# Kernel tuning notes

Measured on AMD Instinct MI355X. Metric: run time of the kernel, lower is better.

## Reference

```python
import jax, jax.numpy as jnp
import numpy as np

BITWIDTH = 8
T = 1 << BITWIDTH  # 256 bit-clock cycles
N = 262144         # independent bitstreams


def _sobol_1d(dim, n=T, out_bits=BITWIDTH):
    """One coordinate of an n-point Sobol sequence (Joe-Kuo dirs), scaled to [0, 2^out_bits)."""
    L = 30
    if dim == 1:
        v = [1 << (L - 1 - j) for j in range(L)]  # van der Corput
    else:
        params = {2: (1, 0, [1]), 3: (2, 1, [1, 3]), 4: (3, 1, [1, 3, 1])}
        s, a, m = params[dim]
        vv = [0] * (L + 1)
        for j in range(1, s + 1):
            vv[j] = m[j - 1] << (L - j)
        for j in range(s + 1, L + 1):
            vj = vv[j - s] ^ (vv[j - s] >> s)
            for k in range(1, s):
                if (a >> (s - 1 - k)) & 1:
                    vj ^= vv[j - k]
            vv[j] = vj
        v = vv[1:]
    x = np.zeros(n, dtype=np.int64)
    for i in range(1, n):
        acc, ii, j = 0, i, 0
        while ii:
            if ii & 1:
                acc ^= v[j]
            ii >>= 1
            j += 1
        x[i] = acc
    return (x >> (L - out_bits)).astype(np.float32)  # integers in [0, 256)


def _const_bitstream(value, rng_dim):
    """BSGen(SourceGen(value)): bit[t] = (round(value*2^B) > sobol_rng[t])."""
    src = np.round(value * (1 << BITWIDTH)).astype(np.float32)
    rng = _sobol_1d(rng_dim)
    return jnp.asarray((src > rng).astype(np.float32))


def setup_inputs() -> dict:
    key = jax.random.key(0)
    # input bitstream: Bernoulli bits (probability 0.5), one row per bit-clock
    x = jax.random.bernoulli(key, 0.5, (T, N)).astype(jnp.float32)
    return {
        "x": x,
        "c2": _const_bitstream(62.0 / 153.0, 1),  # rng_dim + 0
        "c3": _const_bitstream(17.0 / 42.0, 2),   # rng_dim + 1
        "c4": _const_bitstream(2.0 / 5.0, 3),     # rng_dim + 2
        "c5": _const_bitstream(1.0 / 3.0, 4),     # rng_dim + 3
    }


def reference(x, c2, c3, c4, c5):
    """tanhP1 combinational unary tanh over a T-cycle bitstream, vectorized over N.
    Bits are {0,1} floats: AND == multiply, NOT == 1 - (.)."""
    n = x.shape[1]

    def step(carry, inp):
        in_d, n1_d = carry              # in_d: [8,N] (d1..d8), n1_d: [3,N] (d1..d3)
        xt, b2, b3, b4, b5 = inp
        n1 = xt * in_d[3]               # input & input_d4
        n2 = 1.0 - n1 * b2
        n3 = 1.0 - n2 * b3 * n1_d[0]
        n4 = 1.0 - n3 * b4 * n1_d[1]
        n5 = 1.0 - n4 * b5 * n1_d[2]
        out = n5 * in_d[7]              # n_5 & input_d8
        in_d = jnp.concatenate([xt[None], in_d[:7]], axis=0)
        n1_d = jnp.concatenate([n1[None], n1_d[:2]], axis=0)
        return (in_d, n1_d), out

    in_d0 = jnp.zeros((8, n), x.dtype)
    n1_d0 = jnp.zeros((3, n), x.dtype)
    _, ys = jax.lax.scan(step, (in_d0, n1_d0), (x, c2, c3, c4, c5))
    return ys  # [T, N] output bitstream
```

## Files before the change

### kernel.cpp

```cpp
#include <hip/hip_runtime.h>

#define TSTEPS 256
#define CHUNK  64

__device__ __forceinline__ float4 f4mul(const float4 a, const float4 b) {
    return make_float4(a.x * b.x, a.y * b.y, a.z * b.z, a.w * b.w);
}
__device__ __forceinline__ float4 f4nandm(const float4 a, const float b, const float4 m) {
    return make_float4(1.f - a.x * b * m.x, 1.f - a.y * b * m.y,
                       1.f - a.z * b * m.z, 1.f - a.w * b * m.w);
}

__global__ __launch_bounds__(256) void tanhP1_kernel(
    const float* __restrict__ x,
    const float* __restrict__ c2, const float* __restrict__ c3,
    const float* __restrict__ c4, const float* __restrict__ c5,
    float* __restrict__ out, int N4)
{
    __shared__ float sb2[TSTEPS], sb3[TSTEPS], sb4[TSTEPS], sb5[TSTEPS];
    const int tid = threadIdx.x;
    if (tid < TSTEPS) {
        sb2[tid] = c2[tid]; sb3[tid] = c3[tid];
        sb4[tid] = c4[tid]; sb5[tid] = c5[tid];
    }
    __syncthreads();

    const int j4 = blockIdx.x * blockDim.x + tid;
    if (j4 >= N4) return;
    const int t0 = blockIdx.y * CHUNK;

    const float4* __restrict__ x4   = (const float4*)x;
    float4* __restrict__       out4 = (float4*)out;

    float4 xd[8];
    float4 m[3];

    if (t0 == 0) {
        #pragma unroll
        for (int k = 0; k < 8; ++k) xd[k] = make_float4(0.f, 0.f, 0.f, 0.f);
        #pragma unroll
        for (int k = 0; k < 3; ++k) m[k] = make_float4(0.f, 0.f, 0.f, 0.f);
    } else {
        #pragma unroll
        for (int k = 0; k < 8; ++k)
            xd[k] = x4[(size_t)(t0 - 1 - k) * N4 + j4];
        #pragma unroll
        for (int k = 0; k < 3; ++k)
            m[k] = f4mul(xd[k], xd[k + 4]);
    }

    #pragma unroll 8
    for (int t = t0; t < t0 + CHUNK; ++t) {
        const float4 xt = x4[(size_t)t * N4 + j4];
        const float b2 = sb2[t], b3 = sb3[t], b4 = sb4[t], b5 = sb5[t];

        const float4 n1 = f4mul(xt, xd[3]);
        const float4 n2 = make_float4(1.f - n1.x * b2, 1.f - n1.y * b2,
                                      1.f - n1.z * b2, 1.f - n1.w * b2);
        const float4 n3 = f4nandm(n2, b3, m[0]);
        const float4 n4 = f4nandm(n3, b4, m[1]);
        const float4 n5 = f4nandm(n4, b5, m[2]);

        out4[(size_t)t * N4 + j4] = f4mul(n5, xd[7]);

        xd[7] = xd[6]; xd[6] = xd[5]; xd[5] = xd[4]; xd[4] = xd[3];
        xd[3] = xd[2]; xd[2] = xd[1]; xd[1] = xd[0]; xd[0] = xt;
        m[2] = m[1]; m[1] = m[0]; m[0] = n1;
    }
}

extern "C" void kernel_launch(void* const* d_in, const int* in_sizes, int n_in,
                              void* d_out, int out_size, void* d_ws, size_t ws_size,
                              hipStream_t stream) {
    const float* x  = (const float*)d_in[0];
    const float* c2 = (const float*)d_in[1];
    const float* c3 = (const float*)d_in[2];
    const float* c4 = (const float*)d_in[3];
    const float* c5 = (const float*)d_in[4];
    float* out = (float*)d_out;

    const int N  = in_sizes[0] / TSTEPS;
    const int N4 = N / 4;

    dim3 block(256);
    dim3 grid((N4 + 255) / 256, TSTEPS / CHUNK);
    tanhP1_kernel<<<grid, block, 0, stream>>>(x, c2, c3, c4, c5, out, N4);
}
```

Measured before the change: 443.1 us.

## Batch loads in groups of eight, pack constants, use nontemporal stores

Each group of eight time steps now issues all of its loads before computing, and the eight results are written at the end with nontemporal stores, so more memory requests are in flight and output bypasses cache. The four constant streams are packed into one float4 shared array, and the time chunk is doubled so fewer blocks recompute the warmup history. The larger chunk halves the blocks along the time axis, which lowers parallelism and raises register pressure from holding grouped arrays.

```diff
diff --git a/kernel.cpp b/kernel.cpp
--- a/kernel.cpp
+++ b/kernel.cpp
@@ -1,7 +1,10 @@
 #include <hip/hip_runtime.h>
 
 #define TSTEPS 256
-#define CHUNK  64
+#define CHUNK  128
+#define GROUP  8
+
+typedef float v4f __attribute__((ext_vector_type(4)));
 
 __device__ __forceinline__ float4 f4mul(const float4 a, const float4 b) {
     return make_float4(a.x * b.x, a.y * b.y, a.z * b.z, a.w * b.w);
@@ -17,20 +20,19 @@
     const float* __restrict__ c4, const float* __restrict__ c5,
     float* __restrict__ out, int N4)
 {
-    __shared__ float sb2[TSTEPS], sb3[TSTEPS], sb4[TSTEPS], sb5[TSTEPS];
+    __shared__ float4 sbc[TSTEPS];
     const int tid = threadIdx.x;
-    if (tid < TSTEPS) {
-        sb2[tid] = c2[tid]; sb3[tid] = c3[tid];
-        sb4[tid] = c4[tid]; sb5[tid] = c5[tid];
-    }
+    if (tid < TSTEPS)
+        sbc[tid] = make_float4(c2[tid], c3[tid], c4[tid], c5[tid]);
     __syncthreads();
 
     const int j4 = blockIdx.x * blockDim.x + tid;
     if (j4 >= N4) return;
     const int t0 = blockIdx.y * CHUNK;
 
-    const float4* __restrict__ x4   = (const float4*)x;
-    float4* __restrict__       out4 = (float4*)out;
+    const float4* __restrict__ x4   = (const float4*)x + j4;
+    float4* __restrict__       out4 = (float4*)out + j4;
+    const size_t stride = (size_t)N4;
 
     float4 xd[8];
     float4 m[3];
@@ -43,29 +45,42 @@
     } else {
         #pragma unroll
         for (int k = 0; k < 8; ++k)
-            xd[k] = x4[(size_t)(t0 - 1 - k) * N4 + j4];
+            xd[k] = x4[(size_t)(t0 - 1 - k) * stride];
         #pragma unroll
         for (int k = 0; k < 3; ++k)
             m[k] = f4mul(xd[k], xd[k + 4]);
     }
 
-    #pragma unroll 8
-    for (int t = t0; t < t0 + CHUNK; ++t) {
-        const float4 xt = x4[(size_t)t * N4 + j4];
-        const float b2 = sb2[t], b3 = sb3[t], b4 = sb4[t], b5 = sb5[t];
+    #pragma unroll 1
+    for (int g = 0; g < CHUNK; g += GROUP) {
+        const size_t base = (size_t)(t0 + g) * stride;
 
-        const float4 n1 = f4mul(xt, xd[3]);
-        const float4 n2 = make_float4(1.f - n1.x * b2, 1.f - n1.y * b2,
-                                      1.f - n1.z * b2, 1.f - n1.w * b2);
-        const float4 n3 = f4nandm(n2, b3, m[0]);
-        const float4 n4 = f4nandm(n3, b4, m[1]);
-        const float4 n5 = f4nandm(n4, b5, m[2]);
+        float4 xt[GROUP];
+        #pragma unroll
+        for (int i = 0; i < GROUP; ++i)
+            xt[i] = x4[base + (size_t)i * stride];
 
-        out4[(size_t)t * N4 + j4] = f4mul(n5, xd[7]);
+        float4 o[GROUP];
+        #pragma unroll
+        for (int i = 0; i < GROUP; ++i) {
+            const float4 c = sbc[t0 + g + i];
+            const float4 n1 = f4mul(xt[i], xd[3]);
+            const float4 n2 = make_float4(1.f - n1.x * c.x, 1.f - n1.y * c.x,
+                                          1.f - n1.z * c.x, 1.f - n1.w * c.x);
+            const float4 n3 = f4nandm(n2, c.y, m[0]);
+            const float4 n4 = f4nandm(n3, c.z, m[1]);
+            const float4 n5 = f4nandm(n4, c.w, m[2]);
+            o[i] = f4mul(n5, xd[7]);
 
-        xd[7] = xd[6]; xd[6] = xd[5]; xd[5] = xd[4]; xd[4] = xd[3];
-        xd[3] = xd[2]; xd[2] = xd[1]; xd[1] = xd[0]; xd[0] = xt;
-        m[2] = m[1]; m[1] = m[0]; m[0] = n1;
+            xd[7] = xd[6]; xd[6] = xd[5]; xd[5] = xd[4]; xd[4] = xd[3];
+            xd[3] = xd[2]; xd[2] = xd[1]; xd[1] = xd[0]; xd[0] = xt[i];
+            m[2] = m[1]; m[1] = m[0]; m[0] = n1;
+        }
+
+        #pragma unroll
+        for (int i = 0; i < GROUP; ++i)
+            __builtin_nontemporal_store(*(const v4f*)&o[i],
+                                        (v4f*)&out4[base + (size_t)i * stride]);
     }
 }
 
```

Result: no change. 450.6 us (+1.7%).
